# Optimization experiments

Measured on AMD Instinct MI355X. Metric: run time of the kernel, lower is better.

## Reference

```python
import jax, jax.numpy as jnp
import numpy as np

NUM_HEADS = 32
NUM_KV_HEADS = 8
HEAD_DIM = 128
SEQ = 2048
MASK_BLOCK = 128  # diffusion-LM denoising block size


def setup_inputs() -> dict:
    key = jax.random.key(0)
    kq, kk, kv = jax.random.split(key, 3)
    q = jax.random.normal(kq, (SEQ, NUM_HEADS * HEAD_DIM), dtype=jnp.float32)
    k = jax.random.normal(kk, (SEQ, NUM_KV_HEADS * HEAD_DIM), dtype=jnp.float32)
    v = jax.random.normal(kv, (SEQ, NUM_KV_HEADS * HEAD_DIM), dtype=jnp.float32)
    # block-causal mask at MASK_BLOCK granularity: token_q attends to token_kv
    # iff block(token_kv) <= block(token_q). Every row has >=1 True entry.
    blk = jnp.arange(SEQ) // MASK_BLOCK
    block_mask = blk[None, :] <= blk[:, None]  # [S, S] bool
    return {"q": q, "k": k, "v": v, "block_mask": block_mask}


def reference(q, k, v, block_mask):
    S = q.shape[0]
    scale = 1.0 / np.sqrt(HEAD_DIM).astype(np.float32)  # flex_attention default scale
    qh = q.reshape(S, NUM_HEADS, HEAD_DIM)       # [S, Hq, D]
    kh = k.reshape(S, NUM_KV_HEADS, HEAD_DIM)    # [S, Hkv, D]
    vh = v.reshape(S, NUM_KV_HEADS, HEAD_DIM)
    # GQA: repeat each kv head over its query-head group
    group = NUM_HEADS // NUM_KV_HEADS
    kh = jnp.repeat(kh, group, axis=1)           # [S, Hq, D]
    vh = jnp.repeat(vh, group, axis=1)
    scores = jnp.einsum('qhd,khd->hqk', qh, kh) * scale  # [Hq, S, S]
    neg_inf = jnp.finfo(scores.dtype).min
    scores = jnp.where(block_mask[None, :, :], scores, neg_inf)
    probs = jax.nn.softmax(scores, axis=-1)
    o = jnp.einsum('hqk,khd->qhd', probs, vh)    # [S, Hq, D]
    return o.reshape(S, NUM_HEADS * HEAD_DIM)
```

## Files before the change

### kernel.cpp

```cpp
#include <hip/hip_runtime.h>
#include <hip/hip_bf16.h>

#define SEQL  2048
#define NHQ   32
#define NHKV  8
#define HD    128

typedef __attribute__((ext_vector_type(4)))  float          f32x4;
typedef __attribute__((ext_vector_type(16))) float          f32x16;
typedef __attribute__((ext_vector_type(8)))  short          bf16x8;
typedef __attribute__((ext_vector_type(4)))  unsigned short u16x4;
typedef __attribute__((ext_vector_type(8)))  unsigned short u16x8;

__device__ __forceinline__ unsigned short f2bf(float f) {
  union { float f; unsigned u; } v; v.f = f;
  unsigned u = v.u;
  return (unsigned short)((u + 0x7fffu + ((u >> 16) & 1u)) >> 16);
}

__device__ __forceinline__ unsigned cvtpk_bf16(float lo, float hi) {
  unsigned r;
  asm("v_cvt_pk_bf16_f32 %0, %1, %2" : "=v"(r) : "v"(lo), "v"(hi));
  return r;
}

__device__ __forceinline__ void gload16(const void* g, void* l) {
  __builtin_amdgcn_global_load_lds(
      (const __attribute__((address_space(1))) unsigned int*)g,
      (__attribute__((address_space(3))) unsigned int*)l, 16, 0, 0);
}

__global__ __launch_bounds__(256) void prep_k(const float* __restrict__ k,
                                              unsigned short* __restrict__ kws) {
  int t = blockIdx.x * 256 + threadIdx.x;
  int s   = t >> 7;
  int col = (t & 127) << 3;
  int hkv = col >> 7;
  int d0  = col & 127;
  const float* src = k + (size_t)s * (NHKV * HD) + col;
  f32x4 a = *(const f32x4*)src;
  f32x4 b = *(const f32x4*)(src + 4);
  u16x8 r;
  r[0] = f2bf(a[0]); r[1] = f2bf(a[1]); r[2] = f2bf(a[2]); r[3] = f2bf(a[3]);
  r[4] = f2bf(b[0]); r[5] = f2bf(b[1]); r[6] = f2bf(b[2]); r[7] = f2bf(b[3]);
  int tile = s >> 6, rr = s & 63;
  int idx = (rr * 128 + d0) ^ ((rr & 7) << 3);
  *(u16x8*)(kws + (((size_t)(hkv * 32 + tile)) << 13) + idx) = r;
}

__global__ __launch_bounds__(256) void prep_v(const float* __restrict__ v,
                                              unsigned short* __restrict__ vws) {
  int t = blockIdx.x * 256 + threadIdx.x;
  int d    = t & 127;
  int hkv  = (t >> 7) & 7;
  int rest = t >> 10;
  int tile = rest >> 3;
  int s    = (rest >> 1) & 3;
  int hh   = rest & 1;
  int s0   = tile * 64 + s * 16 + hh * 4;
  const float* src = v + (size_t)s0 * (NHKV * HD) + hkv * HD + d;
  u16x8 r;
  #pragma unroll
  for (int j = 0; j < 8; ++j) {
    int soff = ((j >> 2) << 3) + (j & 3);
    r[j] = f2bf(src[(size_t)soff * (NHKV * HD)]);
  }
  int idx = (d * 64 + s * 16 + hh * 8) ^ ((d & 7) << 3);
  *(u16x8*)(vws + (((size_t)(hkv * 32 + tile)) << 13) + idx) = r;
}

__global__ __launch_bounds__(128) void attn_fwd14(
    const float* __restrict__ q,
    const unsigned short* __restrict__ kws,
    const unsigned short* __restrict__ vws,
    float* __restrict__ out)
{
  __shared__ unsigned short Kb[2][8192];
  __shared__ unsigned short Vb[2][8192];

  const int tid  = threadIdx.x;
  const int lane = tid & 63;
  const int wv   = tid >> 6;
  const int l31  = lane & 31;
  const int h8   = lane >> 5;

  const int bx   = blockIdx.x;
  const int hkv  = bx & 7;
  const int h    = hkv * 4 + ((bx >> 3) & 3);
  const int pr   = bx >> 5;
  const int qtA  = pr, qtB = 31 - pr;
  const int nA   = ((qtA >> 1) + 1) * 2;
  const int T    = 34;

  const float qscale = 0.08838834764831845f * 1.4426950408889634f;
  const float THR = 11.5f;

  const unsigned short* ktiles = kws + (((size_t)hkv * 32) << 13);
  const unsigned short* vtiles = vws + (((size_t)hkv * 32) << 13);

  bf16x8 qf[8];
  f32x16 oacc[4];
  float mrun, lrun;

  auto loadQ = [&](int qt) {
    const float* qbase = q + (size_t)(qt * 64 + wv * 32 + l31) * (NHQ * HD) + h * HD + h8 * 8;
    #pragma unroll
    for (int c = 0; c < 8; ++c) {
      f32x4 a = *(const f32x4*)(qbase + c * 16);
      f32x4 b = *(const f32x4*)(qbase + c * 16 + 4);
      bf16x8 r;
      r[0] = (short)f2bf(a[0] * qscale);
      r[1] = (short)f2bf(a[1] * qscale);
      r[2] = (short)f2bf(a[2] * qscale);
      r[3] = (short)f2bf(a[3] * qscale);
      r[4] = (short)f2bf(b[0] * qscale);
      r[5] = (short)f2bf(b[1] * qscale);
      r[6] = (short)f2bf(b[2] * qscale);
      r[7] = (short)f2bf(b[3] * qscale);
      qf[c] = r;
    }
  };

  auto resetAcc = [&]() {
    #pragma unroll
    for (int i = 0; i < 4; ++i)
      oacc[i] = (f32x16){0.f,0.f,0.f,0.f,0.f,0.f,0.f,0.f,0.f,0.f,0.f,0.f,0.f,0.f,0.f,0.f};
    mrun = -1e30f; lrun = 0.f;
  };

  auto epilogue = [&](int qt) {
    float invl = 1.0f / lrun;
    float* ob = out + (size_t)(qt * 64 + wv * 32 + l31) * (NHQ * HD) + h * HD + h8 * 4;
    #pragma unroll
    for (int db = 0; db < 4; ++db) {
      #pragma unroll
      for (int rq = 0; rq < 4; ++rq) {
        f32x4 vv;
        vv[0] = oacc[db][4 * rq + 0] * invl;
        vv[1] = oacc[db][4 * rq + 1] * invl;
        vv[2] = oacc[db][4 * rq + 2] * invl;
        vv[3] = oacc[db][4 * rq + 3] * invl;
        *(f32x4*)(ob + db * 32 + rq * 8) = vv;
      }
    }
  };

  auto STAGE = [&](int b, int kvt) {
    const char* gk = (const char*)(ktiles + ((size_t)kvt << 13));
    const char* gv = (const char*)(vtiles + ((size_t)kvt << 13));
    char* lk = (char*)&Kb[b][0];
    char* lv = (char*)&Vb[b][0];
    #pragma unroll
    for (int i = 0; i < 8; ++i) {
      const int off = wv * 8192 + i * 1024;
      gload16(gk + off + lane * 16, lk + off);
      gload16(gv + off + lane * 16, lv + off);
    }
  };

  auto compute = [&](int b) {
    f32x16 s0 = (f32x16){0.f,0.f,0.f,0.f,0.f,0.f,0.f,0.f,0.f,0.f,0.f,0.f,0.f,0.f,0.f,0.f};
    f32x16 s1 = s0;
    __builtin_amdgcn_s_setprio(1);
    #pragma unroll
    for (int c = 0; c < 8; ++c) {
      const int r0 = l31;
      const int r1 = 32 + l31;
      bf16x8 kf0 = *(const bf16x8*)(&Kb[b][(r0 * 128 + c * 16 + h8 * 8) ^ ((r0 & 7) << 3)]);
      bf16x8 kf1 = *(const bf16x8*)(&Kb[b][(r1 * 128 + c * 16 + h8 * 8) ^ ((r1 & 7) << 3)]);
      s0 = __builtin_amdgcn_mfma_f32_32x32x16_bf16(kf0, qf[c], s0, 0, 0, 0);
      s1 = __builtin_amdgcn_mfma_f32_32x32x16_bf16(kf1, qf[c], s1, 0, 0, 0);
    }
    __builtin_amdgcn_s_setprio(0);
    float m0 = fmaxf(fmaxf(s0[0], s0[1]),  fmaxf(s0[2], s0[3]));
    float m1 = fmaxf(fmaxf(s0[4], s0[5]),  fmaxf(s0[6], s0[7]));
    float m2 = fmaxf(fmaxf(s0[8], s0[9]),  fmaxf(s0[10], s0[11]));
    float m3 = fmaxf(fmaxf(s0[12], s0[13]), fmaxf(s0[14], s0[15]));
    float m4 = fmaxf(fmaxf(s1[0], s1[1]),  fmaxf(s1[2], s1[3]));
    float m5 = fmaxf(fmaxf(s1[4], s1[5]),  fmaxf(s1[6], s1[7]));
    float m6 = fmaxf(fmaxf(s1[8], s1[9]),  fmaxf(s1[10], s1[11]));
    float m7 = fmaxf(fmaxf(s1[12], s1[13]), fmaxf(s1[14], s1[15]));
    float mt = fmaxf(fmaxf(fmaxf(m0, m1), fmaxf(m2, m3)),
                     fmaxf(fmaxf(m4, m5), fmaxf(m6, m7)));
    mt = fmaxf(mt, __shfl_xor(mt, 32));
    if (__any(mt > mrun + THR)) {
      float mn = fmaxf(mrun, mt);
      float c0 = exp2f(mrun - mn);
      mrun = mn; lrun *= c0;
      #pragma unroll
      for (int i = 0; i < 4; ++i) oacc[i] *= c0;
    }
    unsigned pw[16];
    float ts = 0.f;
    #pragma unroll
    for (int i = 0; i < 8; ++i) {
      float p0 = exp2f(s0[2 * i]     - mrun);
      float p1 = exp2f(s0[2 * i + 1] - mrun);
      ts += p0 + p1;
      pw[i] = cvtpk_bf16(p0, p1);
    }
    #pragma unroll
    for (int i = 0; i < 8; ++i) {
      float p0 = exp2f(s1[2 * i]     - mrun);
      float p1 = exp2f(s1[2 * i + 1] - mrun);
      ts += p0 + p1;
      pw[8 + i] = cvtpk_bf16(p0, p1);
    }
    ts += __shfl_xor(ts, 32);
    lrun += ts;
    __builtin_amdgcn_s_setprio(1);
    #pragma unroll
    for (int db = 0; db < 4; ++db) {
      const int d = db * 32 + l31;
      f32x16 acc = oacc[db];
      #pragma unroll
      for (int s = 0; s < 4; ++s) {
        bf16x8 vf = *(const bf16x8*)(&Vb[b][(d * 64 + s * 16 + h8 * 8) ^ ((d & 7) << 3)]);
        union { unsigned u[4]; bf16x8 v8; } pk;
        pk.u[0] = pw[4 * s + 0];
        pk.u[1] = pw[4 * s + 1];
        pk.u[2] = pw[4 * s + 2];
        pk.u[3] = pw[4 * s + 3];
        acc = __builtin_amdgcn_mfma_f32_32x32x16_bf16(vf, pk.v8, acc, 0, 0, 0);
      }
      oacc[db] = acc;
    }
    __builtin_amdgcn_s_setprio(0);
  };

  loadQ(qtA);
  resetAcc();
  STAGE(0, 0);
  int buf = 0;
  #pragma unroll 1
  for (int t = 0; t < T; ++t) {
    if (t == nA) { epilogue(qtA); loadQ(qtB); resetAcc(); }
    if (t + 1 < T) {
      const int p = t + 1;
      STAGE(buf ^ 1, (p < nA) ? p : p - nA);
      asm volatile("s_waitcnt vmcnt(16)" ::: "memory");
    } else {
      asm volatile("s_waitcnt vmcnt(0)" ::: "memory");
    }
    __builtin_amdgcn_s_barrier();
    asm volatile("" ::: "memory");
    compute(buf);
    asm volatile("" ::: "memory");
    __builtin_amdgcn_s_barrier();
    buf ^= 1;
  }
  epilogue(qtB);
}

__global__ __launch_bounds__(256) void attn_v1(
    const float* __restrict__ q,
    const float* __restrict__ k,
    const float* __restrict__ v,
    float* __restrict__ out)
{
  __shared__ unsigned short Ks[64 * 128];
  __shared__ unsigned short Vt[128 * 64];
  __shared__ unsigned short Psl[4][16 * 64];

  const int tid  = threadIdx.x;
  const int lane = tid & 63;
  const int wv   = tid >> 6;
  const int bx   = blockIdx.x;
  const int h    = bx & 31;
  const int qt   = (SEQL / 64 - 1) - (bx >> 5);
  const int q0   = qt * 64;
  const int hkv  = h >> 2;
  const int l15 = lane & 15;
  const int lhi = lane >> 4;
  const float qscale = 0.08838834764831845f * 1.4426950408889634f;

  bf16x8 qf[4];
  {
    const float* qbase = q + (size_t)(q0 + wv * 16 + l15) * (NHQ * HD) + h * HD + lhi * 8;
    #pragma unroll
    for (int c = 0; c < 4; ++c) {
      const float* p8 = qbase + c * 32;
      f32x4 a = *(const f32x4*)p8;
      f32x4 b = *(const f32x4*)(p8 + 4);
      bf16x8 r;
      r[0] = (short)f2bf(a[0] * qscale); r[1] = (short)f2bf(a[1] * qscale);
      r[2] = (short)f2bf(a[2] * qscale); r[3] = (short)f2bf(a[3] * qscale);
      r[4] = (short)f2bf(b[0] * qscale); r[5] = (short)f2bf(b[1] * qscale);
      r[6] = (short)f2bf(b[2] * qscale); r[7] = (short)f2bf(b[3] * qscale);
      qf[c] = r;
    }
  }
  f32x4 oacc[8];
  #pragma unroll
  for (int i = 0; i < 8; ++i) oacc[i] = (f32x4){0.f, 0.f, 0.f, 0.f};
  float mrun[4], lrun[4];
  #pragma unroll
  for (int r = 0; r < 4; ++r) { mrun[r] = -1e30f; lrun[r] = 0.f; }
  const int ntiles = ((q0 >> 7) + 1) * 2;
  for (int t = 0; t < ntiles; ++t) {
    const int kv0 = t * 64;
    __syncthreads();
    #pragma unroll
    for (int it = 0; it < 8; ++it) {
      int c = it * 256 + tid;
      int row = c >> 5;
      int dc = (c & 31) << 2;
      f32x4 x = *(const f32x4*)(k + (size_t)(kv0 + row) * (NHKV * HD) + hkv * HD + dc);
      u16x4 y;
      y[0] = f2bf(x[0]); y[1] = f2bf(x[1]); y[2] = f2bf(x[2]); y[3] = f2bf(x[3]);
      int idx = (row * HD + dc) ^ ((row & 7) << 3);
      *(u16x4*)(&Ks[idx]) = y;
    }
    {
      int row = tid >> 2;
      int db = (tid & 3) << 5;
      const float* vbase = v + (size_t)(kv0 + row) * (NHKV * HD) + hkv * HD + db;
      #pragma unroll
      for (int it = 0; it < 8; ++it) {
        f32x4 x = *(const f32x4*)(vbase + it * 4);
        int d0 = db + it * 4;
        #pragma unroll
        for (int j = 0; j < 4; ++j) {
          int d = d0 + j;
          int idx = (d * 64 + row) ^ ((d & 7) << 3);
          Vt[idx] = f2bf(x[j]);
        }
      }
    }
    __syncthreads();
    f32x4 sacc[4];
    #pragma unroll
    for (int sub = 0; sub < 4; ++sub) {
      f32x4 acc = (f32x4){0.f, 0.f, 0.f, 0.f};
      #pragma unroll
      for (int c = 0; c < 4; ++c) {
        int row = sub * 16 + l15;
        int idx = (row * HD + c * 32 + lhi * 8) ^ ((row & 7) << 3);
        bf16x8 kf = *(const bf16x8*)(&Ks[idx]);
        acc = __builtin_amdgcn_mfma_f32_16x16x32_bf16(qf[c], kf, acc, 0, 0, 0);
      }
      sacc[sub] = acc;
    }
    float corr[4];
    #pragma unroll
    for (int r = 0; r < 4; ++r) {
      float mt = fmaxf(fmaxf(sacc[0][r], sacc[1][r]), fmaxf(sacc[2][r], sacc[3][r]));
      #pragma unroll
      for (int off = 1; off < 16; off <<= 1) mt = fmaxf(mt, __shfl_xor(mt, off));
      float mnew = fmaxf(mrun[r], mt);
      corr[r] = exp2f(mrun[r] - mnew);
      mrun[r] = mnew;
      float p0 = exp2f(sacc[0][r] - mnew);
      float p1 = exp2f(sacc[1][r] - mnew);
      float p2 = exp2f(sacc[2][r] - mnew);
      float p3 = exp2f(sacc[3][r] - mnew);
      int qr = (lhi << 2) + r;
      int swz = (qr & 7) << 3;
      int bq = qr * 64;
      Psl[wv][(bq + 0  + l15) ^ swz] = f2bf(p0);
      Psl[wv][(bq + 16 + l15) ^ swz] = f2bf(p1);
      Psl[wv][(bq + 32 + l15) ^ swz] = f2bf(p2);
      Psl[wv][(bq + 48 + l15) ^ swz] = f2bf(p3);
      float ts = p0 + p1 + p2 + p3;
      #pragma unroll
      for (int off = 1; off < 16; off <<= 1) ts += __shfl_xor(ts, off);
      lrun[r] = lrun[r] * corr[r] + ts;
    }
    #pragma unroll
    for (int dsub = 0; dsub < 8; ++dsub) {
      f32x4 o = oacc[dsub];
      o[0] *= corr[0]; o[1] *= corr[1]; o[2] *= corr[2]; o[3] *= corr[3];
      oacc[dsub] = o;
    }
    #pragma unroll
    for (int kc = 0; kc < 2; ++kc) {
      int pidx = (l15 * 64 + kc * 32 + lhi * 8) ^ ((l15 & 7) << 3);
      bf16x8 pf = *(const bf16x8*)(&Psl[wv][pidx]);
      #pragma unroll
      for (int dsub = 0; dsub < 8; ++dsub) {
        int d = dsub * 16 + l15;
        int vidx = (d * 64 + kc * 32 + lhi * 8) ^ ((d & 7) << 3);
        bf16x8 vf = *(const bf16x8*)(&Vt[vidx]);
        oacc[dsub] = __builtin_amdgcn_mfma_f32_16x16x32_bf16(pf, vf, oacc[dsub], 0, 0, 0);
      }
    }
  }
  float inv[4];
  #pragma unroll
  for (int r = 0; r < 4; ++r) inv[r] = 1.0f / lrun[r];
  float* obase = out + (size_t)(q0 + wv * 16 + (lhi << 2)) * (NHQ * HD) + h * HD + l15;
  #pragma unroll
  for (int dsub = 0; dsub < 8; ++dsub) {
    #pragma unroll
    for (int r = 0; r < 4; ++r) {
      obase[(size_t)r * (NHQ * HD) + dsub * 16] = oacc[dsub][r] * inv[r];
    }
  }
}

extern "C" void kernel_launch(void* const* d_in, const int* in_sizes, int n_in,
                              void* d_out, int out_size, void* d_ws, size_t ws_size,
                              hipStream_t stream) {
  const float* q = (const float*)d_in[0];
  const float* k = (const float*)d_in[1];
  const float* v = (const float*)d_in[2];
  float* out = (float*)d_out;
  const size_t prepNeed = (size_t)8 * 1024 * 1024 + 512;
  if (ws_size >= prepNeed) {
    unsigned short* kws = (unsigned short*)d_ws;
    unsigned short* vws = kws + (size_t)4 * 1024 * 1024 / 2;
    prep_k<<<1024, 256, 0, stream>>>(k, kws);
    prep_v<<<1024, 256, 0, stream>>>(v, vws);
    attn_fwd14<<<512, 128, 0, stream>>>(q, kws, vws, out);
  } else {
    attn_v1<<<1024, 256, 0, stream>>>(q, k, v, out);
  }
}
```

Baseline: 97.51 us.

## Process paired query tiles concurrently in 4-wave blocks sharing staged KV tiles

```diff
diff --git a/kernel.cpp b/kernel.cpp
--- a/kernel.cpp
+++ b/kernel.cpp
@@ -69,7 +69,7 @@
   *(u16x8*)(vws + (((size_t)(hkv * 32 + tile)) << 13) + idx) = r;
 }
 
-__global__ __launch_bounds__(128) void attn_fwd14(
+__global__ __launch_bounds__(256, 2) void attn_fwd15(
     const float* __restrict__ q,
     const unsigned short* __restrict__ kws,
     const unsigned short* __restrict__ vws,
@@ -87,10 +87,14 @@
   const int bx   = blockIdx.x;
   const int hkv  = bx & 7;
   const int h    = hkv * 4 + ((bx >> 3) & 3);
-  const int pr   = bx >> 5;
+  const int idx2 = bx >> 5;
+  const int pr   = (idx2 < 8) ? idx2 : (23 - idx2);
   const int qtA  = pr, qtB = 31 - pr;
   const int nA   = ((qtA >> 1) + 1) * 2;
-  const int T    = 34;
+  const int nB   = ((qtB >> 1) + 1) * 2;
+
+  const int qt   = (wv < 2) ? qtA : qtB;
+  const int nt   = (wv < 2) ? nA  : nB;
 
   const float qscale = 0.08838834764831845f * 1.4426950408889634f;
   const float THR = 11.5f;
@@ -100,10 +104,10 @@
 
   bf16x8 qf[8];
   f32x16 oacc[4];
-  float mrun, lrun;
-
-  auto loadQ = [&](int qt) {
-    const float* qbase = q + (size_t)(qt * 64 + wv * 32 + l31) * (NHQ * HD) + h * HD + h8 * 8;
+  float mrun = -1e30f, lrun = 0.f;
+
+  {
+    const float* qbase = q + (size_t)(qt * 64 + (wv & 1) * 32 + l31) * (NHQ * HD) + h * HD + h8 * 8;
     #pragma unroll
     for (int c = 0; c < 8; ++c) {
       f32x4 a = *(const f32x4*)(qbase + c * 16);
@@ -119,31 +123,10 @@
       r[7] = (short)f2bf(b[3] * qscale);
       qf[c] = r;
     }
-  };
-
-  auto resetAcc = [&]() {
-    #pragma unroll
-    for (int i = 0; i < 4; ++i)
-      oacc[i] = (f32x16){0.f,0.f,0.f,0.f,0.f,0.f,0.f,0.f,0.f,0.f,0.f,0.f,0.f,0.f,0.f,0.f};
-    mrun = -1e30f; lrun = 0.f;
-  };
-
-  auto epilogue = [&](int qt) {
-    float invl = 1.0f / lrun;
-    float* ob = out + (size_t)(qt * 64 + wv * 32 + l31) * (NHQ * HD) + h * HD + h8 * 4;
-    #pragma unroll
-    for (int db = 0; db < 4; ++db) {
-      #pragma unroll
-      for (int rq = 0; rq < 4; ++rq) {
-        f32x4 vv;
-        vv[0] = oacc[db][4 * rq + 0] * invl;
-        vv[1] = oacc[db][4 * rq + 1] * invl;
-        vv[2] = oacc[db][4 * rq + 2] * invl;
-        vv[3] = oacc[db][4 * rq + 3] * invl;
-        *(f32x4*)(ob + db * 32 + rq * 8) = vv;
-      }
-    }
-  };
+  }
+  #pragma unroll
+  for (int i = 0; i < 4; ++i)
+    oacc[i] = (f32x16){0.f,0.f,0.f,0.f,0.f,0.f,0.f,0.f,0.f,0.f,0.f,0.f,0.f,0.f,0.f,0.f};
 
   auto STAGE = [&](int b, int kvt) {
     const char* gk = (const char*)(ktiles + ((size_t)kvt << 13));
@@ -151,8 +134,8 @@
     char* lk = (char*)&Kb[b][0];
     char* lv = (char*)&Vb[b][0];
     #pragma unroll
-    for (int i = 0; i < 8; ++i) {
-      const int off = wv * 8192 + i * 1024;
+    for (int i = 0; i < 4; ++i) {
+      const int off = wv * 4096 + i * 1024;
       gload16(gk + off + lane * 16, lk + off);
       gload16(gv + off + lane * 16, lv + off);
     }
@@ -228,28 +211,40 @@
     __builtin_amdgcn_s_setprio(0);
   };
 
-  loadQ(qtA);
-  resetAcc();
   STAGE(0, 0);
   int buf = 0;
   #pragma unroll 1
-  for (int t = 0; t < T; ++t) {
-    if (t == nA) { epilogue(qtA); loadQ(qtB); resetAcc(); }
-    if (t + 1 < T) {
-      const int p = t + 1;
-      STAGE(buf ^ 1, (p < nA) ? p : p - nA);
-      asm volatile("s_waitcnt vmcnt(16)" ::: "memory");
+  for (int t = 0; t < nB; ++t) {
+    if (t + 1 < nB) {
+      STAGE(buf ^ 1, t + 1);
+      asm volatile("s_waitcnt vmcnt(8)" ::: "memory");
     } else {
       asm volatile("s_waitcnt vmcnt(0)" ::: "memory");
     }
     __builtin_amdgcn_s_barrier();
     asm volatile("" ::: "memory");
-    compute(buf);
+    if (t < nt) compute(buf);
     asm volatile("" ::: "memory");
     __builtin_amdgcn_s_barrier();
     buf ^= 1;
   }
-  epilogue(qtB);
+
+  {
+    float invl = 1.0f / lrun;
+    float* ob = out + (size_t)(qt * 64 + (wv & 1) * 32 + l31) * (NHQ * HD) + h * HD + h8 * 4;
+    #pragma unroll
+    for (int db = 0; db < 4; ++db) {
+      #pragma unroll
+      for (int rq = 0; rq < 4; ++rq) {
+        f32x4 vv;
+        vv[0] = oacc[db][4 * rq + 0] * invl;
+        vv[1] = oacc[db][4 * rq + 1] * invl;
+        vv[2] = oacc[db][4 * rq + 2] * invl;
+        vv[3] = oacc[db][4 * rq + 3] * invl;
+        *(f32x4*)(ob + db * 32 + rq * 8) = vv;
+      }
+    }
+  }
 }
 
 __global__ __launch_bounds__(256) void attn_v1(
@@ -411,7 +406,7 @@
     unsigned short* vws = kws + (size_t)4 * 1024 * 1024 / 2;
     prep_k<<<1024, 256, 0, stream>>>(k, kws);
     prep_v<<<1024, 256, 0, stream>>>(v, vws);
-    attn_fwd14<<<512, 128, 0, stream>>>(q, kws, vws, out);
+    attn_fwd15<<<512, 256, 0, stream>>>(q, kws, vws, out);
   } else {
     attn_v1<<<1024, 256, 0, stream>>>(q, k, v, out);
   }
```

Measured after the change: 88.22 us. -9.5%, faster.
